# Optimization experiments

Measured on AMD Instinct MI355X. Metric: run time of the kernel, lower is better.

The kernel has to match this reference:

```python
import jax, jax.numpy as jnp
import numpy as np

N, M, C, CSKIP, K = 16384, 4096, 256, 128, 3
BIG = 1e10  # distance penalty for cross-batch pairs


def setup_inputs() -> dict:
    key = jax.random.key(0)
    ks = jax.random.split(key, 6)
    return {
        "x": jax.random.normal(ks[0], (M, C), jnp.float32),
        "pos": jax.random.normal(ks[1], (M, 3), jnp.float32),
        "batch": jnp.zeros((M,), jnp.int32),
        "x_skip": jax.random.normal(ks[2], (N, CSKIP), jnp.float32),
        "pos_skip": jax.random.normal(ks[3], (N, 3), jnp.float32),
        "batch_skip": jnp.zeros((N,), jnp.int32),
        "W1": jax.random.normal(ks[4], (C + CSKIP, 256), jnp.float32) * (1.0 / np.sqrt(C + CSKIP)),
        "b1": jnp.zeros((256,), jnp.float32),
        "W2": jax.random.normal(ks[5], (256, 256), jnp.float32) * (1.0 / np.sqrt(256)),
        "b2": jnp.zeros((256,), jnp.float32),
    }


def _knn_idx(pos, pos_skip, batch, batch_skip, k):
    # Squared distances via GEMM form: [N, M]
    a2 = jnp.sum(pos_skip * pos_skip, axis=-1, keepdims=True)      # [N,1]
    b2 = jnp.sum(pos * pos, axis=-1)[None, :]                       # [1,M]
    d2 = a2 + b2 - 2.0 * (pos_skip @ pos.T)                         # [N,M]
    d2 = jnp.where(batch_skip[:, None] != batch[None, :], BIG, d2)
    _, idx = jax.lax.top_k(-d2, k)                                  # [N,k]
    return idx


def reference(x, pos, batch, x_skip, pos_skip, batch_skip, W1, b1, W2, b2):
    idx = _knn_idx(pos, pos_skip, batch, batch_skip, K)             # [N,k] coarse neighbor ids
    # Exact squared dist recomputed from gathered positions (matches torch diff path)
    diff = pos_skip[:, None, :] - pos[idx]                          # [N,k,3]
    d2 = jnp.sum(diff * diff, axis=-1, keepdims=True)               # [N,k,1]
    w = 1.0 / (d2 + 1e-8)                                           # inverse-distance weights
    wsum = jnp.sum(w, axis=1, keepdims=True)                        # per-row scatter_add == sum over k
    w = w / (wsum + 1e-8)
    x_interp = jnp.sum(w * x[idx], axis=1)                          # [N,C]
    h = jnp.concatenate([x_interp, x_skip], axis=1)                 # [N,C+C']
    h = jax.nn.relu(h @ W1 + b1)
    h = jax.nn.relu(h @ W2 + b2)
    return h
```

## Files before the change

### kernel.cpp

```cpp
#include <hip/hip_runtime.h>

typedef float     f4   __attribute__((ext_vector_type(4)));
typedef float     f32x4 __attribute__((ext_vector_type(4)));
typedef _Float16  h8   __attribute__((ext_vector_type(8)));
typedef _Float16  h4   __attribute__((ext_vector_type(4)));
typedef _Float16  h2   __attribute__((ext_vector_type(2)));

#define NQ   16384
#define MP   4096
#define CF   256
#define CSK  128
#define K1   384
#define HID  256
#define QB   16
#define MB   64

__device__ __forceinline__ unsigned umed3(unsigned a, unsigned b, unsigned c) {
    unsigned r;
    asm("v_med3_u32 %0, %1, %2, %3" : "=v"(r) : "v"(a), "v"(b), "v"(c));
    return r;
}

__global__ __launch_bounds__(256) void wconv_kernel(
    const float* __restrict__ W1, const float* __restrict__ W2,
    _Float16* __restrict__ Wt1, _Float16* __restrict__ Wt2)
{
    const int i = blockIdx.x * 256 + threadIdx.x;
    if (i < K1 * HID) {
        const int k = i >> 8, n = i & 255;
        Wt1[(size_t)(k >> 5) * 8192 + ((k >> 3) & 3) * 2048 + n * 8 + (k & 7)]
            = (_Float16)W1[i];
    } else {
        const int i2 = i - K1 * HID;
        const int k = i2 >> 8, n = i2 & 255;
        Wt2[(size_t)(k >> 5) * 8192 + ((k >> 3) & 3) * 2048 + n * 8 + (k & 7)]
            = (_Float16)W2[i2];
    }
}

__global__ __launch_bounds__(256, 4) void knn_kernel(
    const float* __restrict__ pos,
    const float* __restrict__ pos_skip,
    unsigned short* __restrict__ fidx_g,
    float* __restrict__ fw_g)
{
    __shared__ __align__(16) char smem[26112];
    _Float16* pxh = (_Float16*)smem;
    _Float16* pyh = (_Float16*)(smem + 8192);
    _Float16* pzh = (_Float16*)(smem + 16384);
    unsigned short (*ci)[48] = (unsigned short (*)[48])(smem + 24576);

    const int tid = threadIdx.x;

    {
        const f4* posv = (const f4*)pos;
        for (int m = tid; m < MP / 4; m += 256) {
            const f4 a = posv[3*m], b = posv[3*m+1], c = posv[3*m+2];
            h4 hx, hy, hz;
            hx[0]=(_Float16)a[0]; hx[1]=(_Float16)a[3];
            hx[2]=(_Float16)b[2]; hx[3]=(_Float16)c[1];
            hy[0]=(_Float16)a[1]; hy[1]=(_Float16)b[0];
            hy[2]=(_Float16)b[3]; hy[3]=(_Float16)c[2];
            hz[0]=(_Float16)a[2]; hz[1]=(_Float16)b[1];
            hz[2]=(_Float16)c[0]; hz[3]=(_Float16)c[3];
            *(h4*)&pxh[4*m] = hx;
            *(h4*)&pyh[4*m] = hy;
            *(h4*)&pzh[4*m] = hz;
        }
    }
    __syncthreads();

    const int lane = tid & 63;
    const int wv   = tid >> 6;

    {
        h2 q2x[4], q2y[4], q2z[4];
        #pragma unroll
        for (int k = 0; k < 4; k++) {
            const int q = blockIdx.x * QB + wv * 4 + k;
            const _Float16 hx = (_Float16)pos_skip[3*q+0];
            const _Float16 hy = (_Float16)pos_skip[3*q+1];
            const _Float16 hz = (_Float16)pos_skip[3*q+2];
            q2x[k][0] = hx; q2x[k][1] = hx;
            q2y[k][0] = hy; q2y[k][1] = hy;
            q2z[k][0] = hz; q2z[k][1] = hz;
        }

        unsigned K0[4], K1v[4], K2[4];
        #pragma unroll
        for (int k = 0; k < 4; k++) { K0[k] = ~0u; K1v[k] = ~0u; K2[k] = ~0u; }

        #define INS(k, key) {                                              \
            const unsigned o0 = K0[k], o1 = K1v[k], o2 = K2[k];            \
            K0[k]  = min(o0, (key));                                       \
            K1v[k] = umed3(o0, o1, (key));                                 \
            K2[k]  = umed3(o1, o2, (key));                                 \
        }

        union hpack { h4 v4; h2 v2[2]; };
        #define EVALP(CX, CY, CZ, JB)                                      \
            _Pragma("unroll")                                              \
            for (int k = 0; k < 4; k++) {                                  \
                _Pragma("unroll")                                          \
                for (int pp = 0; pp < 2; pp++) {                           \
                    const h2 dx = q2x[k] - (CX).v2[pp];                    \
                    const h2 dy = q2y[k] - (CY).v2[pp];                    \
                    const h2 dz = q2z[k] - (CZ).v2[pp];                    \
                    const h2 dd = dx*dx + dy*dy + dz*dz;                   \
                    const unsigned du = __builtin_bit_cast(unsigned, dd);  \
                    const unsigned key0 = ((du & 0xFFFFu) << 12) + (JB) + pp*2; \
                    const unsigned key1 = ((du >> 16) << 12) + (JB) + pp*2 + 1; \
                    INS(k, key0);                                          \
                    INS(k, key1);                                          \
                }                                                          \
            }

        const h4* px4 = (const h4*)pxh;
        const h4* py4 = (const h4*)pyh;
        const h4* pz4 = (const h4*)pzh;

        hpack cx, cy, cz, nx, ny, nz;
        int idx = lane;
        cx.v4 = px4[idx]; cy.v4 = py4[idx]; cz.v4 = pz4[idx];

        for (int it = 0; it < 16; ++it) {
            const int nidx = idx + 64;
            nx.v4 = px4[nidx]; ny.v4 = py4[nidx]; nz.v4 = pz4[nidx];
            const unsigned jb = (unsigned)(it * 256 + lane * 4);
            EVALP(cx, cy, cz, jb);
            cx = nx; cy = ny; cz = nz;
            idx = nidx;
        }
        #undef EVALP
        #undef INS

        #pragma unroll
        for (int k = 0; k < 4; k++) {
            unsigned a0 = K0[k], a1 = K1v[k], a2 = K2[k];
            {
                const unsigned b0 = (unsigned)__builtin_amdgcn_ds_swizzle((int)a0, 0x041F);
                const unsigned b1 = (unsigned)__builtin_amdgcn_ds_swizzle((int)a1, 0x041F);
                const unsigned b2 = (unsigned)__builtin_amdgcn_ds_swizzle((int)a2, 0x041F);
                const unsigned m0 = min(a0, b0);
                const unsigned c1 = max(a0, b0);
                const unsigned d0 = min(a1, b1), d1 = max(a1, b1);
                const unsigned m1 = min(c1, d0);
                const unsigned m2 = min(min(max(c1, d0), d1), min(a2, b2));
                a0 = m0; a1 = m1; a2 = m2;
            }
            {
                const unsigned b0 = (unsigned)__builtin_amdgcn_ds_swizzle((int)a0, 0x081F);
                const unsigned b1 = (unsigned)__builtin_amdgcn_ds_swizzle((int)a1, 0x081F);
                const unsigned b2 = (unsigned)__builtin_amdgcn_ds_swizzle((int)a2, 0x081F);
                const unsigned m0 = min(a0, b0);
                const unsigned c1 = max(a0, b0);
                const unsigned d0 = min(a1, b1), d1 = max(a1, b1);
                const unsigned m1 = min(c1, d0);
                const unsigned m2 = min(min(max(c1, d0), d1), min(a2, b2));
                a0 = m0; a1 = m1; a2 = m2;
            }
            if (!(lane & 3)) {
                const int q = wv * 4 + k;
                const int pr = lane >> 2;
                ci[q][pr*3+0] = (unsigned short)(a0 & 0xFFFu);
                ci[q][pr*3+1] = (unsigned short)(a1 & 0xFFFu);
                ci[q][pr*3+2] = (unsigned short)(a2 & 0xFFFu);
            }
        }
    }
    __syncthreads();

    if (tid < 8 * QB) {
        const int q    = tid >> 3;
        const int part = tid & 7;
        const int g    = blockIdx.x * QB + q;
        const double qxd = (double)pos_skip[3*g+0];
        const double qyd = (double)pos_skip[3*g+1];
        const double qzd = (double)pos_skip[3*g+2];
        const double a2d = qxd*qxd + qyd*qyd + qzd*qzd;

        double e0 = 1e300, e1 = 1e300, e2 = 1e300;
        int    j0 = 0,     j1 = 0,     j2 = 0;
        #pragma unroll
        for (int c = 0; c < 6; c++) {
            const int j = ci[q][part*6 + c];
            const double pxd = (double)pos[3*j+0];
            const double pyd = (double)pos[3*j+1];
            const double pzd = (double)pos[3*j+2];
            const double b2  = pxd*pxd + pyd*pyd + pzd*pzd;
            const double dot = qxd*pxd + qyd*pyd + qzd*pzd;
            const double d   = (a2d + b2) - 2.0 * dot;
            if (d < e2) {
                if (d < e1) {
                    e2 = e1; j2 = j1;
                    if (d < e0) { e1 = e0; j1 = j0; e0 = d; j0 = j; }
                    else        { e1 = d;  j1 = j; }
                } else { e2 = d; j2 = j; }
            }
        }
        ci[q][part*3+0] = (unsigned short)j0;
        ci[q][part*3+1] = (unsigned short)j1;
        ci[q][part*3+2] = (unsigned short)j2;
    }
    __syncthreads();

    if (tid < QB) {
        const int g = blockIdx.x * QB + tid;
        const double qxd = (double)pos_skip[3*g+0];
        const double qyd = (double)pos_skip[3*g+1];
        const double qzd = (double)pos_skip[3*g+2];
        const double a2d = qxd*qxd + qyd*qyd + qzd*qzd;

        double e0 = 1e300, e1 = 1e300, e2 = 1e300;
        int    j0 = 0,     j1 = 0,     j2 = 0;
        for (int p = 0; p < 8; p++) {
            #pragma unroll
            for (int s = 0; s < 3; s++) {
                const int j = ci[tid][p*3+s];
                const double pxd = (double)pos[3*j+0];
                const double pyd = (double)pos[3*j+1];
                const double pzd = (double)pos[3*j+2];
                const double b2  = pxd*pxd + pyd*pyd + pzd*pzd;
                const double dot = qxd*pxd + qyd*pyd + qzd*pzd;
                const double d   = (a2d + b2) - 2.0 * dot;
                if (d < e2) {
                    if (d < e1) {
                        e2 = e1; j2 = j1;
                        if (d < e0) { e1 = e0; j1 = j0; e0 = d; j0 = j; }
                        else        { e1 = d;  j1 = j; }
                    } else { e2 = d; j2 = j; }
                }
            }
        }
        const float sx = pos_skip[3*g+0], sy = pos_skip[3*g+1], sz = pos_skip[3*g+2];
        const int jj[3] = { j0, j1, j2 };
        float wv3[3];
        #pragma unroll
        for (int k = 0; k < 3; k++) {
            const float dx = sx - pos[3*jj[k]+0];
            const float dy = sy - pos[3*jj[k]+1];
            const float dz = sz - pos[3*jj[k]+2];
            const float dd = dx*dx + dy*dy + dz*dz;
            wv3[k] = 1.0f / (dd + 1e-8f);
        }
        const float inv = 1.0f / (wv3[0] + wv3[1] + wv3[2] + 1e-8f);
        #pragma unroll
        for (int k = 0; k < 3; k++) {
            fidx_g[g*3+k] = (unsigned short)jj[k];
            fw_g[g*3+k]   = wv3[k] * inv;
        }
    }
}

__global__ __launch_bounds__(256, 2) void mlp_kernel(
    const float* __restrict__ x,
    const float* __restrict__ x_skip,
    const _Float16* __restrict__ Wt1,
    const _Float16* __restrict__ Wt2,
    const float* __restrict__ b1,
    const float* __restrict__ b2,
    const unsigned short* __restrict__ fidx_g,
    const float* __restrict__ fw_g,
    float* __restrict__ out)
{
    __shared__ __align__(16) char smem[50176];
    _Float16 (*As)[392] = (_Float16 (*)[392])smem;
    _Float16 (*Hs)[264] = (_Float16 (*)[264])smem;

    const int tid  = threadIdx.x;
    const int row0 = blockIdx.x * MB;

    {
        const int r   = tid >> 2;
        const int sub = tid & 3;
        const int g   = row0 + r;
        const int j0 = fidx_g[g*3+0], j1 = fidx_g[g*3+1], j2 = fidx_g[g*3+2];
        const float w0 = fw_g[g*3+0], w1 = fw_g[g*3+1], w2 = fw_g[g*3+2];
        const f4* xa = (const f4*)(x + (size_t)j0 * CF);
        const f4* xb = (const f4*)(x + (size_t)j1 * CF);
        const f4* xc = (const f4*)(x + (size_t)j2 * CF);
        const f4* xs = (const f4*)(x_skip + (size_t)g * CSK);
        #pragma unroll
        for (int t = 0; t < 16; t++) {
            const int c4 = t * 4 + sub;
            const f4 a = xa[c4], b = xb[c4], c = xc[c4];
            const f4 v = a * w0 + b * w1 + c * w2;
            h4 hv; hv[0]=(_Float16)v[0]; hv[1]=(_Float16)v[1];
                   hv[2]=(_Float16)v[2]; hv[3]=(_Float16)v[3];
            *(h4*)&As[r][c4 * 4] = hv;
        }
        #pragma unroll
        for (int t = 0; t < 8; t++) {
            const int c4 = t * 4 + sub;
            const f4 v = xs[c4];
            h4 hv; hv[0]=(_Float16)v[0]; hv[1]=(_Float16)v[1];
                   hv[2]=(_Float16)v[2]; hv[3]=(_Float16)v[3];
            *(h4*)&As[r][CF + c4 * 4] = hv;
        }
    }

    const int ln   = tid & 15;
    const int quad = (tid >> 4) & 3;
    const int wv   = tid >> 6;
    const int nb   = wv * 64;
    const int q8   = quad * 8;

    const _Float16* w1b = Wt1 + quad * 2048 + (size_t)(nb + ln) * 8;
    const _Float16* w2b = Wt2 + quad * 2048 + (size_t)(nb + ln) * 8;

    f32x4 acc[4][4];
    #pragma unroll
    for (int rg = 0; rg < 4; rg++)
        #pragma unroll
        for (int nt = 0; nt < 4; nt++) acc[rg][nt] = (f32x4)0.0f;

    h8 B[2][4];
    #pragma unroll
    for (int s = 0; s < 2; s++)
        #pragma unroll
        for (int nt = 0; nt < 4; nt++)
            B[s][nt] = *(const h8*)(w1b + (size_t)s * 8192 + nt * 128);

    __syncthreads();

    #pragma unroll
    for (int kb = 0; kb < 12; kb++) {
        const int s = kb & 1;
        h8 hb[4];
        #pragma unroll
        for (int nt = 0; nt < 4; nt++) hb[nt] = B[s][nt];
        const int nk = kb + 2;
        if (nk < 12) {
            #pragma unroll
            for (int nt = 0; nt < 4; nt++)
                B[s][nt] = *(const h8*)(w1b + (size_t)nk * 8192 + nt * 128);
        } else {
            #pragma unroll
            for (int nt = 0; nt < 4; nt++)
                B[s][nt] = *(const h8*)(w2b + (size_t)(nk - 12) * 8192 + nt * 128);
        }
        #pragma unroll
        for (int rg = 0; rg < 4; rg++) {
            const h8 ha = *(const h8*)&As[rg * 16 + ln][kb * 32 + q8];
            #pragma unroll
            for (int nt = 0; nt < 4; nt++)
                acc[rg][nt] = __builtin_amdgcn_mfma_f32_16x16x32_f16(ha, hb[nt], acc[rg][nt], 0, 0, 0);
        }
    }
    __syncthreads();

    #pragma unroll
    for (int nt = 0; nt < 4; nt++) {
        const int n = nb + nt * 16 + ln;
        const float bv = b1[n];
        #pragma unroll
        for (int rg = 0; rg < 4; rg++) {
            #pragma unroll
            for (int r = 0; r < 4; r++) {
                Hs[rg * 16 + quad * 4 + r][n] =
                    (_Float16)fmaxf(acc[rg][nt][r] + bv, 0.0f);
            }
            acc[rg][nt] = (f32x4)0.0f;
        }
    }
    __syncthreads();

    #pragma unroll
    for (int kb = 0; kb < 8; kb++) {
        const int s = kb & 1;
        h8 hb[4];
        #pragma unroll
        for (int nt = 0; nt < 4; nt++) hb[nt] = B[s][nt];
        const int nk = kb + 2;
        if (nk < 8) {
            #pragma unroll
            for (int nt = 0; nt < 4; nt++)
                B[s][nt] = *(const h8*)(w2b + (size_t)nk * 8192 + nt * 128);
        }
        #pragma unroll
        for (int rg = 0; rg < 4; rg++) {
            const h8 ha = *(const h8*)&Hs[rg * 16 + ln][kb * 32 + q8];
            #pragma unroll
            for (int nt = 0; nt < 4; nt++)
                acc[rg][nt] = __builtin_amdgcn_mfma_f32_16x16x32_f16(ha, hb[nt], acc[rg][nt], 0, 0, 0);
        }
    }

    #pragma unroll
    for (int nt = 0; nt < 4; nt++) {
        const int n = nb + nt * 16 + ln;
        const float bv = b2[n];
        #pragma unroll
        for (int rg = 0; rg < 4; rg++) {
            #pragma unroll
            for (int r = 0; r < 4; r++) {
                const int m = rg * 16 + quad * 4 + r;
                out[(size_t)(row0 + m) * HID + n] = fmaxf(acc[rg][nt][r] + bv, 0.0f);
            }
        }
    }
}

extern "C" void kernel_launch(void* const* d_in, const int* in_sizes, int n_in,
                              void* d_out, int out_size, void* d_ws, size_t ws_size,
                              hipStream_t stream) {
    const float* x         = (const float*)d_in[0];
    const float* pos       = (const float*)d_in[1];
    const float* x_skip    = (const float*)d_in[3];
    const float* pos_skip  = (const float*)d_in[4];
    const float* W1        = (const float*)d_in[6];
    const float* b1        = (const float*)d_in[7];
    const float* W2        = (const float*)d_in[8];
    const float* b2        = (const float*)d_in[9];
    float* out = (float*)d_out;

    char* ws = (char*)d_ws;
    _Float16*       Wt1    = (_Float16*)ws;
    _Float16*       Wt2    = (_Float16*)(ws + 196608);
    unsigned short* fidx_g = (unsigned short*)(ws + 327680);
    float*          fw_g   = (float*)(ws + 425984);

    wconv_kernel<<<(K1*HID + HID*HID) / 256, 256, 0, stream>>>(W1, W2, Wt1, Wt2);
    knn_kernel<<<NQ / QB, 256, 0, stream>>>(pos, pos_skip, fidx_g, fw_g);
    mlp_kernel<<<NQ / MB, 256, 0, stream>>>(x, x_skip, Wt1, Wt2, b1, b2,
                                            fidx_g, fw_g, out);
}
```

Measured before the change: 126.8 us.

## Fuse KNN and MLP kernels into one 512-thread block per 64 queries

Merges the KNN search kernel and the MLP kernel into a single kernel. Each 512-thread block handles 64 query rows, keeping neighbor indices and weights in shared memory instead of a global workspace. This removes one launch and the global round-trip for idx and weights. It also amortizes the per-block staging of the 4096 fp16 point positions over 64 queries instead of 16. In exchange each wave now tracks 8 queries in registers and the MLP tiles are split across 8 waves, which may raise register pressure and lower occupancy.

Result: faster. 123.6 us (-2.5%).

```diff
diff --git a/kernel.cpp b/kernel.cpp
--- a/kernel.cpp
+++ b/kernel.cpp
@@ -12,8 +12,7 @@
 #define CSK  128
 #define K1   384
 #define HID  256
-#define QB   16
-#define MB   64
+#define QBK  64
 
 __device__ __forceinline__ unsigned umed3(unsigned a, unsigned b, unsigned c) {
     unsigned r;
@@ -38,23 +37,32 @@
     }
 }
 
-__global__ __launch_bounds__(256, 4) void knn_kernel(
+__global__ __launch_bounds__(512, 2) void fused_kernel(
     const float* __restrict__ pos,
     const float* __restrict__ pos_skip,
-    unsigned short* __restrict__ fidx_g,
-    float* __restrict__ fw_g)
+    const float* __restrict__ x,
+    const float* __restrict__ x_skip,
+    const _Float16* __restrict__ Wt1,
+    const _Float16* __restrict__ Wt2,
+    const float* __restrict__ b1,
+    const float* __restrict__ b2,
+    float* __restrict__ out)
 {
-    __shared__ __align__(16) char smem[26112];
+    __shared__ __align__(16) char smem[51712];
     _Float16* pxh = (_Float16*)smem;
     _Float16* pyh = (_Float16*)(smem + 8192);
     _Float16* pzh = (_Float16*)(smem + 16384);
     unsigned short (*ci)[48] = (unsigned short (*)[48])(smem + 24576);
+    _Float16 (*As)[392] = (_Float16 (*)[392])smem;
+    _Float16 (*Hs)[264] = (_Float16 (*)[264])smem;
+    int   (*fidx)[3] = (int (*)[3])(smem + 50176);
+    float (*fw)[3]   = (float (*)[3])(smem + 50944);
 
     const int tid = threadIdx.x;
 
     {
         const f4* posv = (const f4*)pos;
-        for (int m = tid; m < MP / 4; m += 256) {
+        for (int m = tid; m < MP / 4; m += 512) {
             const f4 a = posv[3*m], b = posv[3*m+1], c = posv[3*m+2];
             h4 hx, hy, hz;
             hx[0]=(_Float16)a[0]; hx[1]=(_Float16)a[3];
@@ -74,10 +82,10 @@
     const int wv   = tid >> 6;
 
     {
-        h2 q2x[4], q2y[4], q2z[4];
-        #pragma unroll
-        for (int k = 0; k < 4; k++) {
-            const int q = blockIdx.x * QB + wv * 4 + k;
+        h2 q2x[8], q2y[8], q2z[8];
+        #pragma unroll
+        for (int k = 0; k < 8; k++) {
+            const int q = blockIdx.x * QBK + wv * 8 + k;
             const _Float16 hx = (_Float16)pos_skip[3*q+0];
             const _Float16 hy = (_Float16)pos_skip[3*q+1];
             const _Float16 hz = (_Float16)pos_skip[3*q+2];
@@ -86,9 +94,9 @@
             q2z[k][0] = hz; q2z[k][1] = hz;
         }
 
-        unsigned K0[4], K1v[4], K2[4];
-        #pragma unroll
-        for (int k = 0; k < 4; k++) { K0[k] = ~0u; K1v[k] = ~0u; K2[k] = ~0u; }
+        unsigned K0[8], K1v[8], K2[8];
+        #pragma unroll
+        for (int k = 0; k < 8; k++) { K0[k] = ~0u; K1v[k] = ~0u; K2[k] = ~0u; }
 
         #define INS(k, key) {                                              \
             const unsigned o0 = K0[k], o1 = K1v[k], o2 = K2[k];            \
@@ -100,7 +108,7 @@
         union hpack { h4 v4; h2 v2[2]; };
         #define EVALP(CX, CY, CZ, JB)                                      \
             _Pragma("unroll")                                              \
-            for (int k = 0; k < 4; k++) {                                  \
+            for (int k = 0; k < 8; k++) {                                  \
                 _Pragma("unroll")                                          \
                 for (int pp = 0; pp < 2; pp++) {                           \
                     const h2 dx = q2x[k] - (CX).v2[pp];                    \
@@ -135,7 +143,7 @@
         #undef INS
 
         #pragma unroll
-        for (int k = 0; k < 4; k++) {
+        for (int k = 0; k < 8; k++) {
             unsigned a0 = K0[k], a1 = K1v[k], a2 = K2[k];
             {
                 const unsigned b0 = (unsigned)__builtin_amdgcn_ds_swizzle((int)a0, 0x041F);
@@ -160,7 +168,7 @@
                 a0 = m0; a1 = m1; a2 = m2;
             }
             if (!(lane & 3)) {
-                const int q = wv * 4 + k;
+                const int q = wv * 8 + k;
                 const int pr = lane >> 2;
                 ci[q][pr*3+0] = (unsigned short)(a0 & 0xFFFu);
                 ci[q][pr*3+1] = (unsigned short)(a1 & 0xFFFu);
@@ -170,10 +178,10 @@
     }
     __syncthreads();
 
-    if (tid < 8 * QB) {
+    {
         const int q    = tid >> 3;
         const int part = tid & 7;
-        const int g    = blockIdx.x * QB + q;
+        const int g    = blockIdx.x * QBK + q;
         const double qxd = (double)pos_skip[3*g+0];
         const double qyd = (double)pos_skip[3*g+1];
         const double qzd = (double)pos_skip[3*g+2];
@@ -204,8 +212,8 @@
     }
     __syncthreads();
 
-    if (tid < QB) {
-        const int g = blockIdx.x * QB + tid;
+    if (tid < QBK) {
+        const int g = blockIdx.x * QBK + tid;
         const double qxd = (double)pos_skip[3*g+0];
         const double qyd = (double)pos_skip[3*g+1];
         const double qzd = (double)pos_skip[3*g+2];
@@ -246,43 +254,27 @@
         const float inv = 1.0f / (wv3[0] + wv3[1] + wv3[2] + 1e-8f);
         #pragma unroll
         for (int k = 0; k < 3; k++) {
-            fidx_g[g*3+k] = (unsigned short)jj[k];
-            fw_g[g*3+k]   = wv3[k] * inv;
-        }
-    }
-}
-
-__global__ __launch_bounds__(256, 2) void mlp_kernel(
-    const float* __restrict__ x,
-    const float* __restrict__ x_skip,
-    const _Float16* __restrict__ Wt1,
-    const _Float16* __restrict__ Wt2,
-    const float* __restrict__ b1,
-    const float* __restrict__ b2,
-    const unsigned short* __restrict__ fidx_g,
-    const float* __restrict__ fw_g,
-    float* __restrict__ out)
-{
-    __shared__ __align__(16) char smem[50176];
-    _Float16 (*As)[392] = (_Float16 (*)[392])smem;
-    _Float16 (*Hs)[264] = (_Float16 (*)[264])smem;
-
-    const int tid  = threadIdx.x;
-    const int row0 = blockIdx.x * MB;
+            fidx[tid][k] = jj[k];
+            fw[tid][k]   = wv3[k] * inv;
+        }
+    }
+    __syncthreads();
+
+    const int row0 = blockIdx.x * QBK;
 
     {
-        const int r   = tid >> 2;
-        const int sub = tid & 3;
+        const int r   = tid >> 3;
+        const int sub = tid & 7;
         const int g   = row0 + r;
-        const int j0 = fidx_g[g*3+0], j1 = fidx_g[g*3+1], j2 = fidx_g[g*3+2];
-        const float w0 = fw_g[g*3+0], w1 = fw_g[g*3+1], w2 = fw_g[g*3+2];
+        const int j0 = fidx[r][0], j1 = fidx[r][1], j2 = fidx[r][2];
+        const float w0 = fw[r][0], w1 = fw[r][1], w2 = fw[r][2];
         const f4* xa = (const f4*)(x + (size_t)j0 * CF);
         const f4* xb = (const f4*)(x + (size_t)j1 * CF);
         const f4* xc = (const f4*)(x + (size_t)j2 * CF);
         const f4* xs = (const f4*)(x_skip + (size_t)g * CSK);
         #pragma unroll
-        for (int t = 0; t < 16; t++) {
-            const int c4 = t * 4 + sub;
+        for (int t = 0; t < 8; t++) {
+            const int c4 = t * 8 + sub;
             const f4 a = xa[c4], b = xb[c4], c = xc[c4];
             const f4 v = a * w0 + b * w1 + c * w2;
             h4 hv; hv[0]=(_Float16)v[0]; hv[1]=(_Float16)v[1];
@@ -290,8 +282,8 @@
             *(h4*)&As[r][c4 * 4] = hv;
         }
         #pragma unroll
-        for (int t = 0; t < 8; t++) {
-            const int c4 = t * 4 + sub;
+        for (int t = 0; t < 4; t++) {
+            const int c4 = t * 8 + sub;
             const f4 v = xs[c4];
             h4 hv; hv[0]=(_Float16)v[0]; hv[1]=(_Float16)v[1];
                    hv[2]=(_Float16)v[2]; hv[3]=(_Float16)v[3];
@@ -301,24 +293,23 @@
 
     const int ln   = tid & 15;
     const int quad = (tid >> 4) & 3;
-    const int wv   = tid >> 6;
-    const int nb   = wv * 64;
+    const int nb   = wv * 32;
     const int q8   = quad * 8;
 
     const _Float16* w1b = Wt1 + quad * 2048 + (size_t)(nb + ln) * 8;
     const _Float16* w2b = Wt2 + quad * 2048 + (size_t)(nb + ln) * 8;
 
-    f32x4 acc[4][4];
+    f32x4 acc[4][2];
     #pragma unroll
     for (int rg = 0; rg < 4; rg++)
         #pragma unroll
-        for (int nt = 0; nt < 4; nt++) acc[rg][nt] = (f32x4)0.0f;
-
-    h8 B[2][4];
+        for (int nt = 0; nt < 2; nt++) acc[rg][nt] = (f32x4)0.0f;
+
+    h8 B[2][2];
     #pragma unroll
     for (int s = 0; s < 2; s++)
         #pragma unroll
-        for (int nt = 0; nt < 4; nt++)
+        for (int nt = 0; nt < 2; nt++)
             B[s][nt] = *(const h8*)(w1b + (size_t)s * 8192 + nt * 128);
 
     __syncthreads();
@@ -326,31 +317,31 @@
     #pragma unroll
     for (int kb = 0; kb < 12; kb++) {
         const int s = kb & 1;
-        h8 hb[4];
-        #pragma unroll
-        for (int nt = 0; nt < 4; nt++) hb[nt] = B[s][nt];
+        h8 hb[2];
+        #pragma unroll
+        for (int nt = 0; nt < 2; nt++) hb[nt] = B[s][nt];
         const int nk = kb + 2;
         if (nk < 12) {
             #pragma unroll
-            for (int nt = 0; nt < 4; nt++)
+            for (int nt = 0; nt < 2; nt++)
                 B[s][nt] = *(const h8*)(w1b + (size_t)nk * 8192 + nt * 128);
         } else {
             #pragma unroll
-            for (int nt = 0; nt < 4; nt++)
+            for (int nt = 0; nt < 2; nt++)
                 B[s][nt] = *(const h8*)(w2b + (size_t)(nk - 12) * 8192 + nt * 128);
         }
         #pragma unroll
         for (int rg = 0; rg < 4; rg++) {
             const h8 ha = *(const h8*)&As[rg * 16 + ln][kb * 32 + q8];
             #pragma unroll
-            for (int nt = 0; nt < 4; nt++)
+            for (int nt = 0; nt < 2; nt++)
                 acc[rg][nt] = __builtin_amdgcn_mfma_f32_16x16x32_f16(ha, hb[nt], acc[rg][nt], 0, 0, 0);
         }
     }
     __syncthreads();
 
     #pragma unroll
-    for (int nt = 0; nt < 4; nt++) {
+    for (int nt = 0; nt < 2; nt++) {
         const int n = nb + nt * 16 + ln;
         const float bv = b1[n];
         #pragma unroll
@@ -368,26 +359,26 @@
     #pragma unroll
     for (int kb = 0; kb < 8; kb++) {
         const int s = kb & 1;
-        h8 hb[4];
-        #pragma unroll
-        for (int nt = 0; nt < 4; nt++) hb[nt] = B[s][nt];
+        h8 hb[2];
+        #pragma unroll
+        for (int nt = 0; nt < 2; nt++) hb[nt] = B[s][nt];
         const int nk = kb + 2;
         if (nk < 8) {
             #pragma unroll
-            for (int nt = 0; nt < 4; nt++)
+            for (int nt = 0; nt < 2; nt++)
                 B[s][nt] = *(const h8*)(w2b + (size_t)nk * 8192 + nt * 128);
         }
         #pragma unroll
         for (int rg = 0; rg < 4; rg++) {
             const h8 ha = *(const h8*)&Hs[rg * 16 + ln][kb * 32 + q8];
             #pragma unroll
-            for (int nt = 0; nt < 4; nt++)
+            for (int nt = 0; nt < 2; nt++)
                 acc[rg][nt] = __builtin_amdgcn_mfma_f32_16x16x32_f16(ha, hb[nt], acc[rg][nt], 0, 0, 0);
         }
     }
 
     #pragma unroll
-    for (int nt = 0; nt < 4; nt++) {
+    for (int nt = 0; nt < 2; nt++) {
         const int n = nb + nt * 16 + ln;
         const float bv = b2[n];
         #pragma unroll
@@ -415,13 +406,10 @@
     float* out = (float*)d_out;
 
     char* ws = (char*)d_ws;
-    _Float16*       Wt1    = (_Float16*)ws;
-    _Float16*       Wt2    = (_Float16*)(ws + 196608);
-    unsigned short* fidx_g = (unsigned short*)(ws + 327680);
-    float*          fw_g   = (float*)(ws + 425984);
+    _Float16* Wt1 = (_Float16*)ws;
+    _Float16* Wt2 = (_Float16*)(ws + 196608);
 
     wconv_kernel<<<(K1*HID + HID*HID) / 256, 256, 0, stream>>>(W1, W2, Wt1, Wt2);
-    knn_kernel<<<NQ / QB, 256, 0, stream>>>(pos, pos_skip, fidx_g, fw_g);
-    mlp_kernel<<<NQ / MB, 256, 0, stream>>>(x, x_skip, Wt1, Wt2, b1, b2,
-                                            fidx_g, fw_g, out);
+    fused_kernel<<<NQ / QBK, 512, 0, stream>>>(pos, pos_skip, x, x_skip,
+                                               Wt1, Wt2, b1, b2, out);
 }
```
